# Performance work log

Measured on AMD Instinct MI355X. Metric: run time of the kernel, lower is better.

Reference implementation:

```python
import jax, jax.numpy as jnp
import numpy as np


def setup_inputs() -> dict:
    key = jax.random.key(0)
    k1, k2 = jax.random.split(key)
    N, D = 8192, 200
    preds = jax.random.normal(k1, (N, 1, 1, D), dtype=jnp.float32)
    labels = jax.random.randint(k2, (N,), 0, 64, dtype=jnp.int64)
    return {"preds": preds, "labels": labels}


def reference(preds, labels):
    # preds: (N,1,1,200) -> flatten to (N,200); torch.dist is the L2 norm of the
    # elementwise difference over the whole tensor.
    N = preds.shape[0]
    x = preds.reshape(N, -1).astype(jnp.float32)
    sq = jnp.sum(x * x, axis=-1)                      # (N,)
    gram = x @ x.T                                    # (N,N)
    d2 = sq[:, None] + sq[None, :] - 2.0 * gram       # squared pairwise dist
    eye = jnp.eye(N, dtype=bool)
    # keep diagonal out of the sqrt (it is skipped by the i==j continue)
    d2_safe = jnp.where(eye, 1.0, jnp.maximum(d2, 0.0))
    dist = jnp.sqrt(d2_safe)                          # (N,N)
    sign = jnp.where(labels[:, None] == labels[None, :], 1.0, -1.0)
    sign = jnp.where(eye, 0.0, sign)
    # each pred_loss[i] is a (1,1,200) tensor filled with the scalar s_i,
    # so the final mean over the stack equals mean_i(s_i).
    per_i = jnp.sum(sign * dist, axis=1)              # (N,)
    return jnp.mean(per_i)
```

## Files before the change

### kernel.cpp

```cpp
#include <hip/hip_runtime.h>
#include <hip/hip_bf16.h>
#include <hip/hip_fp8.h>

#define N 8192
#define D 200
#define KP 232
#define NSTEP 7
#define NB 64
#define NBLK 512
#define NPART (NBLK * 4)
#define PANEL (128 * KP)

typedef float f32x4 __attribute__((ext_vector_type(4)));
#define AS3 __attribute__((address_space(3)))
#define AS1 __attribute__((address_space(1)))

__global__ __launch_bounds__(256) void prep_kernel(
    const float* __restrict__ x, const int* __restrict__ labels,
    unsigned char* __restrict__ xb, float* __restrict__ sq,
    int* __restrict__ lab) {
  int row = blockIdx.x * 4 + (threadIdx.x >> 6);
  int lane = threadIdx.x & 63;
  const float* xr = x + (size_t)row * D;
  unsigned char* xbr = xb + (size_t)row * KP;
  int k0 = lane * 4;
  float4 f = {0.f, 0.f, 0.f, 0.f};
  if (k0 < D) f = *(const float4*)(xr + k0);
  float s = 0.f;
  unsigned char q[4];
  float ff[4] = {f.x, f.y, f.z, f.w};
#pragma unroll
  for (int c = 0; c < 4; ++c) {
    float v = (k0 + c < D) ? ff[c] : 0.f;
    __hip_fp8_e4m3 h(v);
    q[c] = h.__x;
    float fb = (float)h;
    s += fb * fb;
  }
  if (k0 < KP) *(uchar4*)(xbr + k0) = *(uchar4*)q;
#pragma unroll
  for (int m = 32; m; m >>= 1) s += __shfl_xor(s, m);
  if (lane == 0) {
    sq[row] = s;
    lab[row] = labels[row];
  }
}

__global__ __launch_bounds__(256) void gram_kernel(
    const unsigned char* __restrict__ xb, const float* __restrict__ sq,
    const int* __restrict__ lab, double* __restrict__ partial) {
  __shared__ __align__(16) unsigned char sA[PANEL];
  __shared__ __align__(16) unsigned char sB[PANEL];

  const int t = threadIdx.x;
  const int b = blockIdx.x;
  const int q = b >> 4, s = b & 15;
  const int row2 = 63 - q;
  const int n1 = 64 - q;

  const int wid = t >> 6, lane = t & 63;
  const int col = lane & 15, quad = lane >> 4;
  const int waveM = (wid >> 1) * 64, waveN = (wid & 1) * 64;

  auto stage = [&](const unsigned char* g, unsigned char* sh) {
#pragma unroll
    for (int c = 0; c < 7; ++c) {
      int off = c * 4096 + t * 16;
      __builtin_amdgcn_global_load_lds((const AS1 void*)(g + off),
                                       (AS3 void*)(sh + off), 16, 0, 0);
    }
    if (t < 64) {
      int off = 28672 + t * 16;
      __builtin_amdgcn_global_load_lds((const AS1 void*)(g + off),
                                       (AS3 void*)(sh + off), 16, 0, 0);
    }
  };

  int idx = s;
  int bi = (idx < n1) ? q : row2;
  int bj = (idx < n1) ? q + idx : row2 + (idx - n1);
  stage(xb + (size_t)bi * PANEL, sA);
  stage(xb + (size_t)bj * PANEL, sB);
  __syncthreads();

  float tot = 0.f;
  while (true) {
    f32x4 acc[4][4] = {};
#pragma unroll
    for (int step = 0; step < NSTEP; ++step) {
      long a[4], bf[4];
#pragma unroll
      for (int mi = 0; mi < 4; ++mi)
        a[mi] = *(const long*)(sA + (waveM + mi * 16 + col) * KP + step * 32 + quad * 8);
#pragma unroll
      for (int ni = 0; ni < 4; ++ni)
        bf[ni] = *(const long*)(sB + (waveN + ni * 16 + col) * KP + step * 32 + quad * 8);
#pragma unroll
      for (int mi = 0; mi < 4; ++mi)
#pragma unroll
        for (int ni = 0; ni < 4; ++ni)
          acc[mi][ni] = __builtin_amdgcn_mfma_f32_16x16x32_fp8_fp8(
              a[mi], bf[ni], acc[mi][ni], 0, 0, 0);
    }
    __syncthreads();

    const int nidx = idx + 16;
    const bool more = (nidx < 65);
    int nbi = 0, nbj = 0;
    if (more) {
      nbi = (nidx < n1) ? q : row2;
      nbj = (nidx < n1) ? q + nidx : row2 + (nidx - n1);
      if (nbi != bi) stage(xb + (size_t)nbi * PANEL, sA);
      stage(xb + (size_t)nbj * PANEL, sB);
    }

    const int i0 = bi * 128 + waveM, j0 = bj * 128 + waveN;
    int labj[4];
    float sqj[4];
#pragma unroll
    for (int ni = 0; ni < 4; ++ni) {
      int j = j0 + ni * 16 + col;
      labj[ni] = lab[j];
      sqj[ni] = sq[j];
    }
    float rs = 0.f;
    if (bi != bj) {
#pragma unroll
      for (int mi = 0; mi < 4; ++mi) {
#pragma unroll
        for (int r = 0; r < 4; ++r) {
          int i = i0 + mi * 16 + quad * 4 + r;
          float sqi = sq[i];
          int li = lab[i];
#pragma unroll
          for (int ni = 0; ni < 4; ++ni) {
            float g = acc[mi][ni][r];
            float d2 = fmaxf(fmaf(-2.f, g, sqi + sqj[ni]), 0.f);
            float dist = __builtin_amdgcn_sqrtf(d2);
            rs += (li == labj[ni]) ? dist : -dist;
          }
        }
      }
      tot += 2.f * rs;
    } else {
#pragma unroll
      for (int mi = 0; mi < 4; ++mi) {
#pragma unroll
        for (int r = 0; r < 4; ++r) {
          int i = i0 + mi * 16 + quad * 4 + r;
          float sqi = sq[i];
          int li = lab[i];
#pragma unroll
          for (int ni = 0; ni < 4; ++ni) {
            int j = j0 + ni * 16 + col;
            float g = acc[mi][ni][r];
            float d2 = fmaxf(fmaf(-2.f, g, sqi + sqj[ni]), 0.f);
            float dist = __builtin_amdgcn_sqrtf(d2);
            float c = (li == labj[ni]) ? dist : -dist;
            rs += (i == j) ? 0.f : c;
          }
        }
      }
      tot += rs;
    }

    if (!more) break;
    bi = nbi; bj = nbj; idx = nidx;
    __syncthreads();
  }

#pragma unroll
  for (int m = 32; m; m >>= 1) tot += __shfl_xor(tot, m);
  if (lane == 0) partial[b * 4 + wid] = (double)tot;
}

__global__ __launch_bounds__(256) void reduce_kernel(
    const double* __restrict__ partial, float* __restrict__ out) {
  __shared__ double wsum[4];
  double s = 0.0;
  for (int i = threadIdx.x; i < NPART; i += 256) s += partial[i];
#pragma unroll
  for (int m = 32; m; m >>= 1) s += __shfl_xor(s, m);
  if ((threadIdx.x & 63) == 0) wsum[threadIdx.x >> 6] = s;
  __syncthreads();
  if (threadIdx.x == 0)
    out[0] = (float)((wsum[0] + wsum[1] + wsum[2] + wsum[3]) / (double)N);
}

extern "C" void kernel_launch(void* const* d_in, const int* in_sizes, int n_in,
                              void* d_out, int out_size, void* d_ws, size_t ws_size,
                              hipStream_t stream) {
  const float* x = (const float*)d_in[0];
  const int* labels = (const int*)d_in[1];
  char* ws = (char*)d_ws;
  unsigned char* xb = (unsigned char*)ws;
  float* sq = (float*)(ws + (size_t)N * KP);
  int* lab = (int*)(ws + (size_t)N * KP + (size_t)N * 4);
  double* partial = (double*)(ws + (size_t)N * KP + (size_t)N * 8);
  float* out = (float*)d_out;

  prep_kernel<<<N / 4, 256, 0, stream>>>(x, labels, xb, sq, lab);
  gram_kernel<<<NBLK, 256, 0, stream>>>(xb, sq, lab, partial);
  reduce_kernel<<<1, 256, 0, stream>>>(partial, out);
}
```

Baseline: 83.01 us.

## Keep the A panel in registers, drop its LDS buffer, and stagger tile order

Each wave now loads its A-row fragments straight from global memory into registers (28 longs per lane). It reloads them only when the row block changes, instead of staging the A panel into LDS and re-reading it there every step. This halves shared memory per block, and launch bounds of 3 are set so the block can reach higher occupancy. The tile starting index is also rotated per row group so that concurrent blocks fetch different B panels. In exchange, register pressure rises and the global-to-register A loads must be hidden behind the epilogue.

```diff
diff --git a/kernel.cpp b/kernel.cpp
--- a/kernel.cpp
+++ b/kernel.cpp
@@ -46,41 +46,53 @@
   }
 }
 
-__global__ __launch_bounds__(256) void gram_kernel(
+__global__ __launch_bounds__(256, 3) void gram_kernel(
     const unsigned char* __restrict__ xb, const float* __restrict__ sq,
     const int* __restrict__ lab, double* __restrict__ partial) {
-  __shared__ __align__(16) unsigned char sA[PANEL];
   __shared__ __align__(16) unsigned char sB[PANEL];
 
   const int t = threadIdx.x;
   const int b = blockIdx.x;
-  const int q = b >> 4, s = b & 15;
+  const int q = b >> 4, s0 = b & 15;
   const int row2 = 63 - q;
   const int n1 = 64 - q;
+  const int start = (q + s0) & 15;
 
   const int wid = t >> 6, lane = t & 63;
   const int col = lane & 15, quad = lane >> 4;
   const int waveM = (wid >> 1) * 64, waveN = (wid & 1) * 64;
 
-  auto stage = [&](const unsigned char* g, unsigned char* sh) {
+  auto stage = [&](const unsigned char* g) {
 #pragma unroll
     for (int c = 0; c < 7; ++c) {
       int off = c * 4096 + t * 16;
       __builtin_amdgcn_global_load_lds((const AS1 void*)(g + off),
-                                       (AS3 void*)(sh + off), 16, 0, 0);
+                                       (AS3 void*)(sB + off), 16, 0, 0);
     }
     if (t < 64) {
       int off = 28672 + t * 16;
       __builtin_amdgcn_global_load_lds((const AS1 void*)(g + off),
-                                       (AS3 void*)(sh + off), 16, 0, 0);
+                                       (AS3 void*)(sB + off), 16, 0, 0);
     }
   };
 
-  int idx = s;
+  long af[4][NSTEP];
+  auto load_a = [&](int bi_) {
+#pragma unroll
+    for (int mi = 0; mi < 4; ++mi) {
+      const unsigned char* pr =
+          xb + (size_t)(bi_ * 128 + waveM + mi * 16 + col) * KP + quad * 8;
+#pragma unroll
+      for (int st = 0; st < NSTEP; ++st)
+        af[mi][st] = *(const long*)(pr + st * 32);
+    }
+  };
+
+  int idx = start;
   int bi = (idx < n1) ? q : row2;
   int bj = (idx < n1) ? q + idx : row2 + (idx - n1);
-  stage(xb + (size_t)bi * PANEL, sA);
-  stage(xb + (size_t)bj * PANEL, sB);
+  load_a(bi);
+  stage(xb + (size_t)bj * PANEL);
   __syncthreads();
 
   float tot = 0.f;
@@ -88,10 +100,7 @@
     f32x4 acc[4][4] = {};
 #pragma unroll
     for (int step = 0; step < NSTEP; ++step) {
-      long a[4], bf[4];
-#pragma unroll
-      for (int mi = 0; mi < 4; ++mi)
-        a[mi] = *(const long*)(sA + (waveM + mi * 16 + col) * KP + step * 32 + quad * 8);
+      long bf[4];
 #pragma unroll
       for (int ni = 0; ni < 4; ++ni)
         bf[ni] = *(const long*)(sB + (waveN + ni * 16 + col) * KP + step * 32 + quad * 8);
@@ -100,7 +109,7 @@
 #pragma unroll
         for (int ni = 0; ni < 4; ++ni)
           acc[mi][ni] = __builtin_amdgcn_mfma_f32_16x16x32_fp8_fp8(
-              a[mi], bf[ni], acc[mi][ni], 0, 0, 0);
+              af[mi][step], bf[ni], acc[mi][ni], 0, 0, 0);
     }
     __syncthreads();
 
@@ -110,8 +119,8 @@
     if (more) {
       nbi = (nidx < n1) ? q : row2;
       nbj = (nidx < n1) ? q + nidx : row2 + (nidx - n1);
-      if (nbi != bi) stage(xb + (size_t)nbi * PANEL, sA);
-      stage(xb + (size_t)nbj * PANEL, sB);
+      stage(xb + (size_t)nbj * PANEL);
+      if (nbi != bi) load_a(nbi);
     }
 
     const int i0 = bi * 128 + waveM, j0 = bj * 128 + waveN;
```

Result: slower. 88.97 us (+7.2%).
